# Kernel optimization log

Measured on AMD Instinct MI355X. Metric: run time of the kernel, lower is better.

Reference implementation:

```python
import jax, jax.numpy as jnp
import numpy as np

DIM = 768
HEADS = 12
DIM_HEAD = DIM // HEADS  # 64
INNER = DIM_HEAD * HEADS  # 768
HIDDEN = 4 * DIM  # 3072
N = 31  # num_patches + 1, fixed by Block (num_patches=30)
B = 512
EPS = 1e-5
MASK_VAL = -987654321.0


def layernorm(x, g, b):
    mu = jnp.mean(x, axis=-1, keepdims=True)
    var = jnp.mean(jnp.square(x - mu), axis=-1, keepdims=True)
    return (x - mu) * jax.lax.rsqrt(var + EPS) * g + b


def setup_inputs() -> dict:
    key = jax.random.key(0)
    ks = jax.random.split(key, 12)
    s = 0.02
    return {
        "x": jax.random.normal(ks[0], (B, N, DIM), jnp.float32),
        "ln1_g": jnp.ones((DIM,), jnp.float32),
        "ln1_b": jnp.zeros((DIM,), jnp.float32),
        "w_qkv": jax.random.normal(ks[1], (DIM, 3 * INNER), jnp.float32) * s,
        "scale": jnp.full((HEADS,), DIM_HEAD ** -0.5, jnp.float32),
        "w_o": jax.random.normal(ks[2], (INNER, DIM), jnp.float32) * s,
        "b_o": jnp.zeros((DIM,), jnp.float32),
        "ln2_g": jnp.ones((DIM,), jnp.float32),
        "ln2_b": jnp.zeros((DIM,), jnp.float32),
        "w1": jax.random.normal(ks[3], (DIM, HIDDEN), jnp.float32) * s,
        "b1": jnp.zeros((HIDDEN,), jnp.float32),
        "w2": jax.random.normal(ks[4], (HIDDEN, DIM), jnp.float32) * s,
        "b2": jnp.zeros((DIM,), jnp.float32),
    }


def reference(x, ln1_g, ln1_b, w_qkv, scale, w_o, b_o, ln2_g, ln2_b, w1, b1, w2, b2):
    b, n, _ = x.shape
    # --- LSA attention ---
    h = layernorm(x, ln1_g, ln1_b)
    qkv = h @ w_qkv  # [b, n, 3*inner]
    q, k, v = jnp.split(qkv, 3, axis=-1)
    def split_heads(t):
        return t.reshape(b, n, HEADS, DIM_HEAD).transpose(0, 2, 1, 3)  # b h n d
    q, k, v = split_heads(q), split_heads(k), split_heads(v)
    dots = jnp.einsum('bhid,bhjd->bhij', q, k) * scale[None, :, None, None]
    # diagonal exclusion mask (self-token masked out)
    diag = jnp.eye(n, dtype=bool)
    dots = jnp.where(diag[None, None], MASK_VAL, dots)
    attn = jax.nn.softmax(dots, axis=-1)
    out = jnp.einsum('bhij,bhjd->bhid', attn, v)
    out = out.transpose(0, 2, 1, 3).reshape(b, n, INNER)
    x = x + out @ w_o + b_o
    # --- MLP ---
    h2 = layernorm(x, ln2_g, ln2_b)
    h2 = jax.nn.gelu(h2 @ w1 + b1, approximate=False)
    x = x + h2 @ w2 + b2
    return x
```

## Files before the change

### kernel.cpp

```cpp
#include <hip/hip_runtime.h>
#include <math.h>

#define DIM 768
#define HEADS 12
#define DHEAD 64
#define NTOK 31
#define BATCH 512
#define MTOK (BATCH * NTOK)
#define HIDDEN 3072
#define QKVN 2304
#define MASK_VAL -987654321.0f

typedef short s16x8 __attribute__((ext_vector_type(8)));
typedef float f32x4 __attribute__((ext_vector_type(4)));

static __device__ __forceinline__ float bs2f(unsigned short u) {
  unsigned int x = ((unsigned int)u) << 16;
  return __builtin_bit_cast(float, x);
}
static __device__ __forceinline__ unsigned short f2bs(float f) {
  unsigned int x = __builtin_bit_cast(unsigned int, f);
  x += 0x7fffu + ((x >> 16) & 1u);
  return (unsigned short)(x >> 16);
}

static __device__ __forceinline__ void gload16(const unsigned short* g, unsigned short* l) {
  __builtin_amdgcn_global_load_lds(
      (const __attribute__((address_space(1))) unsigned int*)g,
      (__attribute__((address_space(3))) unsigned int*)l, 16, 0, 0);
}

__global__ __launch_bounds__(256) void transpose_kernel(const float* __restrict__ w,
                                                        unsigned short* __restrict__ wt,
                                                        int K, int N) {
  __shared__ float t[64][65];
  int k0 = blockIdx.y * 64, n0 = blockIdx.x * 64;
  int tid = threadIdx.x;
  int r = tid >> 4, c4 = (tid & 15) * 4;
#pragma unroll
  for (int i = 0; i < 4; ++i) {
    float4 v = *(const float4*)(w + (size_t)(k0 + r + i * 16) * N + n0 + c4);
    t[r + i * 16][c4] = v.x;
    t[r + i * 16][c4 + 1] = v.y;
    t[r + i * 16][c4 + 2] = v.z;
    t[r + i * 16][c4 + 3] = v.w;
  }
  __syncthreads();
#pragma unroll
  for (int i = 0; i < 4; ++i) {
    int n = r + i * 16;
    ushort4 o;
    o.x = f2bs(t[c4 + 0][n]);
    o.y = f2bs(t[c4 + 1][n]);
    o.z = f2bs(t[c4 + 2][n]);
    o.w = f2bs(t[c4 + 3][n]);
    *(ushort4*)(wt + (size_t)(n0 + n) * K + k0 + c4) = o;
  }
}

__global__ __launch_bounds__(256) void ln_kernel(const float* __restrict__ x,
                                                 const float* __restrict__ g,
                                                 const float* __restrict__ bta,
                                                 unsigned short* __restrict__ out) {
  int wid = threadIdx.x >> 6, lane = threadIdx.x & 63;
  size_t row = (size_t)blockIdx.x * 4 + wid;
  const float4* xr = (const float4*)(x + row * DIM);
  float4 v[3];
  v[0] = xr[lane];
  v[1] = xr[lane + 64];
  v[2] = xr[lane + 128];
  float s = 0.f, sq = 0.f;
#pragma unroll
  for (int i = 0; i < 3; ++i) {
    s += v[i].x + v[i].y + v[i].z + v[i].w;
    sq += v[i].x * v[i].x + v[i].y * v[i].y + v[i].z * v[i].z + v[i].w * v[i].w;
  }
#pragma unroll
  for (int off = 32; off; off >>= 1) {
    s += __shfl_xor(s, off);
    sq += __shfl_xor(sq, off);
  }
  float mu = s * (1.f / DIM);
  float var = sq * (1.f / DIM) - mu * mu;
  float rs = rsqrtf(var + 1e-5f);
#pragma unroll
  for (int i = 0; i < 3; ++i) {
    int col = i * 256 + lane * 4;
    float4 gg = *(const float4*)(g + col);
    float4 bb = *(const float4*)(bta + col);
    ushort4 o;
    o.x = f2bs((v[i].x - mu) * rs * gg.x + bb.x);
    o.y = f2bs((v[i].y - mu) * rs * gg.y + bb.y);
    o.z = f2bs((v[i].z - mu) * rs * gg.z + bb.z);
    o.w = f2bs((v[i].w - mu) * rs * gg.w + bb.w);
    *(ushort4*)(out + row * DIM + col) = o;
  }
}

__global__ __launch_bounds__(256) void ln_bf16_kernel(const unsigned short* __restrict__ x,
                                                      const float* __restrict__ g,
                                                      const float* __restrict__ bta,
                                                      unsigned short* __restrict__ out) {
  int wid = threadIdx.x >> 6, lane = threadIdx.x & 63;
  size_t row = (size_t)blockIdx.x * 4 + wid;
  const unsigned short* xr = x + row * DIM;
  float v[12];
#pragma unroll
  for (int i = 0; i < 3; ++i) {
    ushort4 u = *(const ushort4*)(xr + i * 256 + lane * 4);
    v[i * 4 + 0] = bs2f(u.x);
    v[i * 4 + 1] = bs2f(u.y);
    v[i * 4 + 2] = bs2f(u.z);
    v[i * 4 + 3] = bs2f(u.w);
  }
  float s = 0.f, sq = 0.f;
#pragma unroll
  for (int i = 0; i < 12; ++i) {
    s += v[i];
    sq += v[i] * v[i];
  }
#pragma unroll
  for (int off = 32; off; off >>= 1) {
    s += __shfl_xor(s, off);
    sq += __shfl_xor(sq, off);
  }
  float mu = s * (1.f / DIM);
  float var = sq * (1.f / DIM) - mu * mu;
  float rs = rsqrtf(var + 1e-5f);
#pragma unroll
  for (int i = 0; i < 3; ++i) {
    int col = i * 256 + lane * 4;
    float4 gg = *(const float4*)(g + col);
    float4 bb = *(const float4*)(bta + col);
    ushort4 o;
    o.x = f2bs((v[i * 4 + 0] - mu) * rs * gg.x + bb.x);
    o.y = f2bs((v[i * 4 + 1] - mu) * rs * gg.y + bb.y);
    o.z = f2bs((v[i * 4 + 2] - mu) * rs * gg.z + bb.z);
    o.w = f2bs((v[i * 4 + 3] - mu) * rs * gg.w + bb.w);
    *(ushort4*)(out + row * DIM + col) = o;
  }
}


template <int BUF, int MH, int KH, int VM, typename STF>
__device__ __forceinline__ void gphase(const char* aP0, const char* aP1,
                                       const char* bP0, const char* bP1,
                                       s16x8* bk, f32x4 (&acc)[8][4], STF&& stage) {
  const char* aP = BUF ? aP1 : aP0;
  const char* bP = BUF ? bP1 : bP0;
  s16x8 af[4];
  if (MH == 0) {
#pragma unroll
    for (int ni = 0; ni < 4; ++ni)
      bk[ni] = *(const s16x8*)(bP + KH * 16384 + ni * 1024);
  }
#pragma unroll
  for (int mi = 0; mi < 4; ++mi)
    af[mi] = *(const s16x8*)(aP + KH * 16384 + MH * 4096 + mi * 1024);
  stage();
  if (VM == 10) asm volatile("s_waitcnt vmcnt(10)");
  if (VM == 4) asm volatile("s_waitcnt vmcnt(4)");
  if (VM == 0) asm volatile("s_waitcnt vmcnt(0)");
  __builtin_amdgcn_s_barrier();
  asm volatile("s_waitcnt lgkmcnt(0)");
  __builtin_amdgcn_s_setprio(1);
#pragma unroll
  for (int mi = 0; mi < 4; ++mi)
#pragma unroll
    for (int ni = 0; ni < 4; ++ni)
      acc[MH * 4 + mi][ni] =
          __builtin_amdgcn_mfma_f32_16x16x32_bf16(af[mi], bk[ni], acc[MH * 4 + mi][ni], 0, 0, 0);
  __builtin_amdgcn_s_setprio(0);
  __builtin_amdgcn_s_barrier();
}

template <int EPI>
__device__ __forceinline__ void gemm8_body(
    const unsigned short* __restrict__ A, const unsigned short* __restrict__ Bt,
    void* __restrict__ outp, const float* __restrict__ bias,
    const void* __restrict__ resid, int M, int N, int K, int ntn) {
  __shared__ unsigned short lds[65536];
  const char* ldsb = (const char*)lds;
  int tid = threadIdx.x;
  int lane = tid & 63, w = tid >> 6;
  int wm = w >> 2, wn = w & 3;
  int fr = lane & 15, q = lane >> 4;

  int nwg = gridDim.x, orig = blockIdx.x;
  int qd = nwg >> 3, r8 = nwg & 7, xcd = orig & 7, loc = orig >> 3;
  int bid = (xcd < r8 ? xcd * (qd + 1) : r8 * (qd + 1) + (xcd - r8) * qd) + loc;
  int m0 = (bid / ntn) * 256, n0 = (bid % ntn) * 256;

  int rdoff = (q * 16) ^ (((fr >> 1) & 3) << 4);
  const char* aP0 = ldsb + (wm * 128 + fr) * 64 + rdoff;
  const char* aP1 = aP0 + 65536;
  const char* bP0 = ldsb + 32768 + (wn * 64 + fr) * 64 + rdoff;
  const char* bP1 = bP0 + 65536;

  int srow = tid >> 2;
  int seoff = (((tid & 3) ^ ((srow >> 1) & 3))) << 3;
  const char* Ab = (const char*)A + ((size_t)(m0 + srow) * K + seoff) * 2;
  const char* Bb = (const char*)Bt + ((size_t)(n0 + srow) * K + seoff) * 2;
  size_t rstep = (size_t)K * 256;

  auto stg = [&](int mat, int kh, int buf, int tile) {
    const char* gp = (mat ? Bb : Ab) + tile * 128 + kh * 64;
    unsigned short* lp = lds + buf * 32768 + mat * 16384 + kh * 8192 + w * 512;
    gload16((const unsigned short*)gp, lp);
    gload16((const unsigned short*)(gp + rstep), lp + 4096);
  };
  auto nop = [&] {};

  f32x4 acc[8][4] = {};
  s16x8 bk[4];
  int NT = K / 64;

  stg(1, 0, 0, 0);
  stg(0, 0, 0, 0);
  stg(1, 1, 0, 0);
  stg(0, 1, 0, 0);
  stg(1, 0, 1, 1);
  stg(0, 0, 1, 1);
  stg(1, 1, 1, 1);
  asm volatile("s_waitcnt vmcnt(6)");
  __builtin_amdgcn_s_barrier();

  for (int t = 0; t + 3 < NT; t += 2) {
    gphase<0, 0, 0, -1>(aP0, aP1, bP0, bP1, bk, acc, [&] { stg(0, 1, 1, t + 1); });
    gphase<0, 1, 0, 10>(aP0, aP1, bP0, bP1, bk, acc, [&] { stg(1, 0, 0, t + 2); });
    gphase<0, 0, 1, -1>(aP0, aP1, bP0, bP1, bk, acc, [&] { stg(0, 0, 0, t + 2); });
    gphase<0, 1, 1, 10>(aP0, aP1, bP0, bP1, bk, acc, [&] { stg(1, 1, 0, t + 2); });
    gphase<1, 0, 0, -1>(aP0, aP1, bP0, bP1, bk, acc, [&] { stg(0, 1, 0, t + 2); });
    gphase<1, 1, 0, 10>(aP0, aP1, bP0, bP1, bk, acc, [&] { stg(1, 0, 1, t + 3); });
    gphase<1, 0, 1, -1>(aP0, aP1, bP0, bP1, bk, acc, [&] { stg(0, 0, 1, t + 3); });
    gphase<1, 1, 1, 10>(aP0, aP1, bP0, bP1, bk, acc, [&] { stg(1, 1, 1, t + 3); });
  }
  gphase<0, 0, 0, -1>(aP0, aP1, bP0, bP1, bk, acc, [&] { stg(0, 1, 1, NT - 1); });
  gphase<0, 1, 0, -1>(aP0, aP1, bP0, bP1, bk, acc, nop);
  gphase<0, 0, 1, -1>(aP0, aP1, bP0, bP1, bk, acc, nop);
  gphase<0, 1, 1, 4>(aP0, aP1, bP0, bP1, bk, acc, nop);
  gphase<1, 0, 0, -1>(aP0, aP1, bP0, bP1, bk, acc, nop);
  gphase<1, 1, 0, 0>(aP0, aP1, bP0, bP1, bk, acc, nop);
  gphase<1, 0, 1, -1>(aP0, aP1, bP0, bP1, bk, acc, nop);
  gphase<1, 1, 1, -1>(aP0, aP1, bP0, bP1, bk, acc, nop);

#pragma unroll
  for (int am = 0; am < 8; ++am) {
#pragma unroll
    for (int ni = 0; ni < 4; ++ni) {
#pragma unroll
      for (int rr = 0; rr < 4; ++rr) {
        int row = m0 + wm * 128 + am * 16 + q * 4 + rr;
        int col = n0 + wn * 64 + ni * 16 + fr;
        size_t idx = (size_t)row * N + col;
        float v = acc[am][ni][rr];
        if (EPI == 0) {
          ((unsigned short*)outp)[idx] = f2bs(v);
        } else if (EPI == 2) {
          float t = v + bias[col];
          float arg = 1.5957691216f * t * (1.f + 0.044715f * t * t);
          float gl = t * __builtin_amdgcn_rcpf(1.f + __expf(-arg));
          ((unsigned short*)outp)[idx] = f2bs(gl);
        } else if (EPI == 3) {
          float t = v + bias[col] + ((const float*)resid)[idx];
          ((unsigned short*)outp)[idx] = f2bs(t);
        } else {
          float t = v + bias[col] + bs2f(((const unsigned short*)resid)[idx]);
          ((float*)outp)[idx] = t;
        }
      }
    }
  }
}

__global__ __launch_bounds__(512, 2) void gemm_qkv(const unsigned short* A,
                                                   const unsigned short* Bt, void* o,
                                                   const float* b, const void* r, int M,
                                                   int N, int K, int ntn) {
  gemm8_body<0>(A, Bt, o, b, r, M, N, K, ntn);
}
__global__ __launch_bounds__(512, 2) void gemm_proj(const unsigned short* A,
                                                    const unsigned short* Bt, void* o,
                                                    const float* b, const void* r, int M,
                                                    int N, int K, int ntn) {
  gemm8_body<3>(A, Bt, o, b, r, M, N, K, ntn);
}
__global__ __launch_bounds__(512, 2) void gemm_mlp1(const unsigned short* A,
                                                    const unsigned short* Bt, void* o,
                                                    const float* b, const void* r, int M,
                                                    int N, int K, int ntn) {
  gemm8_body<2>(A, Bt, o, b, r, M, N, K, ntn);
}
__global__ __launch_bounds__(512, 2) void gemm_mlp2(const unsigned short* A,
                                                    const unsigned short* Bt, void* o,
                                                    const float* b, const void* r, int M,
                                                    int N, int K, int ntn) {
  gemm8_body<4>(A, Bt, o, b, r, M, N, K, ntn);
}

__global__ __launch_bounds__(256) void attn_mfma_kernel(const unsigned short* __restrict__ qkv,
                                                        const float* __restrict__ scale,
                                                        unsigned short* __restrict__ ao) {
  __shared__ unsigned short Vt[4][64][40];
  __shared__ unsigned short Pl[4][32][32];
  int wid = threadIdx.x >> 6, lane = threadIdx.x & 63;
  int pair = blockIdx.x * 4 + wid;
  int b = pair / HEADS, h = pair % HEADS;
  const unsigned short* base = qkv + (size_t)b * NTOK * QKVN + h * DHEAD;
  const unsigned short* Qp = base;
  const unsigned short* Kp = base + 768;
  const unsigned short* Vp = base + 1536;

  int c = lane & 15, q = lane >> 4;
  int oct = q * 8;

  unsigned short vcol[NTOK];
#pragma unroll
  for (int j = 0; j < NTOK; ++j) vcol[j] = Vp[(size_t)j * QKVN + lane];
#pragma unroll
  for (int j = 0; j < NTOK; ++j) Vt[wid][lane][j] = vcol[j];
  Vt[wid][lane][31] = 0;

  s16x8 kf[2][2] = {{{0}}}, qf[2][2] = {{{0}}};
#pragma unroll
  for (int t = 0; t < 2; ++t) {
    int row = t * 16 + c;
    if (row < NTOK) {
#pragma unroll
      for (int s = 0; s < 2; ++s) {
        kf[t][s] = *(const s16x8*)(Kp + (size_t)row * QKVN + s * 32 + oct);
        qf[t][s] = *(const s16x8*)(Qp + (size_t)row * QKVN + s * 32 + oct);
      }
    }
  }

  f32x4 st[2][2] = {};
#pragma unroll
  for (int jt = 0; jt < 2; ++jt)
#pragma unroll
    for (int it = 0; it < 2; ++it)
#pragma unroll
      for (int s = 0; s < 2; ++s)
        st[jt][it] =
            __builtin_amdgcn_mfma_f32_16x16x32_bf16(kf[jt][s], qf[it][s], st[jt][it], 0, 0, 0);

  float scl = scale[h];
  float p[2][2][4];
#pragma unroll
  for (int it = 0; it < 2; ++it)
#pragma unroll
    for (int jt = 0; jt < 2; ++jt)
#pragma unroll
      for (int r = 0; r < 4; ++r) {
        int j = jt * 16 + 4 * q + r;
        int i = it * 16 + c;
        float v = st[jt][it][r] * scl;
        if (j == 31 || j == i) v = MASK_VAL;
        p[it][jt][r] = v;
      }
#pragma unroll
  for (int it = 0; it < 2; ++it) {
    float m = p[it][0][0];
#pragma unroll
    for (int jt = 0; jt < 2; ++jt)
#pragma unroll
      for (int r = 0; r < 4; ++r) m = fmaxf(m, p[it][jt][r]);
    m = fmaxf(m, __shfl_xor(m, 16));
    m = fmaxf(m, __shfl_xor(m, 32));
    float s = 0.f;
#pragma unroll
    for (int jt = 0; jt < 2; ++jt)
#pragma unroll
      for (int r = 0; r < 4; ++r) {
        float e = __expf(p[it][jt][r] - m);
        p[it][jt][r] = e;
        s += e;
      }
    s += __shfl_xor(s, 16);
    s += __shfl_xor(s, 32);
    float inv = __builtin_amdgcn_rcpf(s);
#pragma unroll
    for (int jt = 0; jt < 2; ++jt)
#pragma unroll
      for (int r = 0; r < 4; ++r) p[it][jt][r] *= inv;
  }
#pragma unroll
  for (int it = 0; it < 2; ++it)
#pragma unroll
    for (int jt = 0; jt < 2; ++jt) {
      unsigned int w0 =
          (unsigned int)f2bs(p[it][jt][0]) | ((unsigned int)f2bs(p[it][jt][1]) << 16);
      unsigned int w1 =
          (unsigned int)f2bs(p[it][jt][2]) | ((unsigned int)f2bs(p[it][jt][3]) << 16);
      uint2 pk = {w0, w1};
      *(uint2*)&Pl[wid][it * 16 + c][jt * 16 + 4 * q] = pk;
    }

  s16x8 pa[2];
#pragma unroll
  for (int it = 0; it < 2; ++it) pa[it] = *(const s16x8*)&Pl[wid][it * 16 + c][oct];
  f32x4 o[2][4];
#pragma unroll
  for (int it = 0; it < 2; ++it)
#pragma unroll
    for (int dt = 0; dt < 4; ++dt) {
      s16x8 vb = *(const s16x8*)&Vt[wid][dt * 16 + c][oct];
      f32x4 z = {0.f, 0.f, 0.f, 0.f};
      o[it][dt] = __builtin_amdgcn_mfma_f32_16x16x32_bf16(pa[it], vb, z, 0, 0, 0);
    }
#pragma unroll
  for (int it = 0; it < 2; ++it)
#pragma unroll
    for (int r = 0; r < 4; ++r) {
      int i = it * 16 + 4 * q + r;
      if (i < NTOK) {
        size_t rowoff = ((size_t)b * NTOK + i) * DIM + h * DHEAD;
#pragma unroll
        for (int dt = 0; dt < 4; ++dt) ao[rowoff + dt * 16 + c] = f2bs(o[it][dt][r]);
      }
    }
}

extern "C" void kernel_launch(void* const* d_in, const int* in_sizes, int n_in,
                              void* d_out, int out_size, void* d_ws, size_t ws_size,
                              hipStream_t stream) {
  (void)in_sizes; (void)n_in; (void)out_size; (void)ws_size;
  const float* x = (const float*)d_in[0];
  const float* ln1_g = (const float*)d_in[1];
  const float* ln1_b = (const float*)d_in[2];
  const float* w_qkv = (const float*)d_in[3];
  const float* scale = (const float*)d_in[4];
  const float* w_o = (const float*)d_in[5];
  const float* b_o = (const float*)d_in[6];
  const float* ln2_g = (const float*)d_in[7];
  const float* ln2_b = (const float*)d_in[8];
  const float* w1 = (const float*)d_in[9];
  const float* b1 = (const float*)d_in[10];
  const float* w2 = (const float*)d_in[11];
  const float* b2 = (const float*)d_in[12];

  char* ws = (char*)d_ws;
  unsigned short* buf1 = (unsigned short*)(ws + 0);
  unsigned short* qkv_bf = (unsigned short*)(ws + 24379392);
  unsigned short* x2 = (unsigned short*)(ws + 24379392);
  unsigned short* g_bf = (unsigned short*)(ws + 97517568);
  unsigned short* wqkvT = (unsigned short*)(ws + 195035136);
  unsigned short* woT = (unsigned short*)(ws + 198574080);
  unsigned short* w1T = (unsigned short*)(ws + 199753728);
  unsigned short* w2T = (unsigned short*)(ws + 204472320);

  transpose_kernel<<<dim3(QKVN / 64, DIM / 64), 256, 0, stream>>>(w_qkv, wqkvT, DIM, QKVN);
  transpose_kernel<<<dim3(DIM / 64, DIM / 64), 256, 0, stream>>>(w_o, woT, DIM, DIM);
  transpose_kernel<<<dim3(HIDDEN / 64, DIM / 64), 256, 0, stream>>>(w1, w1T, DIM, HIDDEN);
  transpose_kernel<<<dim3(DIM / 64, HIDDEN / 64), 256, 0, stream>>>(w2, w2T, HIDDEN, DIM);

  ln_kernel<<<MTOK / 4, 256, 0, stream>>>(x, ln1_g, ln1_b, buf1);
  gemm_qkv<<<(MTOK / 256) * (QKVN / 256), 512, 0, stream>>>(
      buf1, wqkvT, qkv_bf, nullptr, nullptr, MTOK, QKVN, DIM, QKVN / 256);
  attn_mfma_kernel<<<(BATCH * HEADS) / 4, 256, 0, stream>>>(qkv_bf, scale, buf1);
  gemm_proj<<<(MTOK / 256) * (DIM / 256), 512, 0, stream>>>(
      buf1, woT, x2, b_o, x, MTOK, DIM, DIM, DIM / 256);
  ln_bf16_kernel<<<MTOK / 4, 256, 0, stream>>>(x2, ln2_g, ln2_b, buf1);
  gemm_mlp1<<<(MTOK / 256) * (HIDDEN / 256), 512, 0, stream>>>(
      buf1, w1T, g_bf, b1, nullptr, MTOK, HIDDEN, DIM, HIDDEN / 256);
  gemm_mlp2<<<(MTOK / 256) * (DIM / 256), 512, 0, stream>>>(
      g_bf, w2T, (float*)d_out, b2, x2, MTOK, DIM, HIDDEN, DIM / 256);
}
```

Baseline: 342.3 us.

## Add 256x192 tile GEMM kernel for N=768 projection and MLP2 GEMMs

Introduces a new GEMM body with 256x192 output tiles (each of 8 waves covers 128x48) and its own LDS layout, swizzle and staging schedule. It is used for the attention output projection and the second MLP GEMM, both of which have N=768. The aim is better wave quantization across CUs: 62 M-tiles times 4 N-tiles gives 248 workgroups instead of 186. In exchange, each workgroup does less MFMA work per byte of A it loads, and the hand-tuned vmcnt wait pipeline is new and could contain stalls or errors. The epilogue code is also factored into shared helper functions.

Result: faster. 330.3 us (-3.5%).

```diff
diff --git a/kernel.cpp b/kernel.cpp
--- a/kernel.cpp
+++ b/kernel.cpp
@@ -28,6 +28,23 @@
   __builtin_amdgcn_global_load_lds(
       (const __attribute__((address_space(1))) unsigned int*)g,
       (__attribute__((address_space(3))) unsigned int*)l, 16, 0, 0);
+}
+
+static __device__ __forceinline__ float epi_apply(int EPI, float v, int col, size_t idx,
+                                                  const float* bias, const void* resid) {
+  if (EPI == 0) return v;
+  if (EPI == 2) {
+    float t = v + bias[col];
+    float arg = 1.5957691216f * t * (1.f + 0.044715f * t * t);
+    return t * __builtin_amdgcn_rcpf(1.f + __expf(-arg));
+  }
+  if (EPI == 3) return v + bias[col] + ((const float*)resid)[idx];
+  return v + bias[col] + bs2f(((const unsigned short*)resid)[idx]);
+}
+
+static __device__ __forceinline__ void epi_store(int EPI, void* outp, size_t idx, float t) {
+  if (EPI == 4) ((float*)outp)[idx] = t;
+  else ((unsigned short*)outp)[idx] = f2bs(t);
 }
 
 __global__ __launch_bounds__(256) void transpose_kernel(const float* __restrict__ w,
@@ -141,7 +158,6 @@
   }
 }
 
-
 template <int BUF, int MH, int KH, int VM, typename STF>
 __device__ __forceinline__ void gphase(const char* aP0, const char* aP1,
                                        const char* bP0, const char* bP1,
@@ -245,32 +261,134 @@
   gphase<1, 1, 1, -1>(aP0, aP1, bP0, bP1, bk, acc, nop);
 
 #pragma unroll
-  for (int am = 0; am < 8; ++am) {
-#pragma unroll
-    for (int ni = 0; ni < 4; ++ni) {
+  for (int am = 0; am < 8; ++am)
+#pragma unroll
+    for (int ni = 0; ni < 4; ++ni)
+#pragma unroll
+      for (int rr = 0; rr < 4; ++rr) {
+        int row = m0 + wm * 128 + am * 16 + (lane >> 4) * 4 + rr;
+        int col = n0 + wn * 64 + ni * 16 + fr;
+        size_t idx = (size_t)row * N + col;
+        epi_store(EPI, outp, idx, epi_apply(EPI, acc[am][ni][rr], col, idx, bias, resid));
+      }
+}
+
+template <int BUF, int MH, int KH, int VM, typename STF>
+__device__ __forceinline__ void gph192(const char* aB0, const char* bKH0, const char* bKH1,
+                                       s16x8 (&bk)[3], f32x4 (&acc)[8][3], STF&& stage) {
+  const char* aP = aB0 + BUF * 32768 + KH * 16384 + MH * 4096;
+  s16x8 af[4];
+  if (MH == 0) {
+    const char* bp = (KH ? bKH1 : bKH0) + BUF * 24576;
+#pragma unroll
+    for (int ni = 0; ni < 3; ++ni) bk[ni] = *(const s16x8*)(bp + ni * 2048);
+  }
+#pragma unroll
+  for (int mi = 0; mi < 4; ++mi) af[mi] = *(const s16x8*)(aP + mi * 1024);
+  stage();
+  if (VM == 2) asm volatile("s_waitcnt vmcnt(2)");
+  if (VM == 0) asm volatile("s_waitcnt vmcnt(0)");
+  __builtin_amdgcn_s_barrier();
+  asm volatile("s_waitcnt lgkmcnt(0)");
+  __builtin_amdgcn_s_setprio(1);
+#pragma unroll
+  for (int mi = 0; mi < 4; ++mi)
+#pragma unroll
+    for (int ni = 0; ni < 3; ++ni)
+      acc[MH * 4 + mi][ni] =
+          __builtin_amdgcn_mfma_f32_16x16x32_bf16(af[mi], bk[ni], acc[MH * 4 + mi][ni], 0, 0, 0);
+  __builtin_amdgcn_s_setprio(0);
+  __builtin_amdgcn_s_barrier();
+}
+
+template <int EPI>
+__device__ __forceinline__ void gemm192_body(
+    const unsigned short* __restrict__ A, const unsigned short* __restrict__ Bt,
+    void* __restrict__ outp, const float* __restrict__ bias,
+    const void* __restrict__ resid, int M, int N, int K, int ntn) {
+  __shared__ char ldsc[114688];
+  int tid = threadIdx.x;
+  int lane = tid & 63, w = tid >> 6;
+  int wm = w >> 2, wn = w & 3;
+  int fr = lane & 15, q = lane >> 4;
+
+  int nwg = gridDim.x, orig = blockIdx.x;
+  int qd = nwg >> 3, r8 = nwg & 7, xcd = orig & 7, loc = orig >> 3;
+  int bid = (xcd < r8 ? xcd * (qd + 1) : r8 * (qd + 1) + (xcd - r8) * qd) + loc;
+  int m0 = (bid / ntn) * 256, n0 = (bid % ntn) * 192;
+
+  int rdoffA = (q * 16) ^ (((fr >> 1) & 3) << 4);
+  const char* aB0 = ldsc + (wm * 128 + fr) * 64 + rdoffA;
+  int brow0 = wn * 48 + fr;
+  int bsw = brow0 & 7;
+  const char* bBase = ldsc + 65536 + brow0 * 128 + (q ^ (bsw & 3)) * 16;
+  const char* bKH0 = bBase + ((0 ^ (bsw >> 2)) * 64);
+  const char* bKH1 = bBase + ((1 ^ (bsw >> 2)) * 64);
+
+  int srow = tid >> 2;
+  int seoffA = (((tid & 3) ^ ((srow >> 1) & 3))) << 3;
+  const char* Ab = (const char*)A + ((size_t)(m0 + srow) * K + seoffA) * 2;
+  size_t rstep = (size_t)K * 256;
+  auto stgA = [&](int kh, int buf, int tile) {
+    const char* gp = Ab + tile * 128 + kh * 64;
+    unsigned short* lp = (unsigned short*)(ldsc + buf * 32768 + kh * 16384 + w * 1024);
+    gload16((const unsigned short*)gp, lp);
+    gload16((const unsigned short*)(gp + rstep), (unsigned short*)((char*)lp + 8192));
+  };
+  const char* Bb2 = (const char*)Bt +
+                    ((size_t)(n0 + (tid >> 3)) * K + (((tid & 7) ^ ((tid >> 3) & 7)) * 8)) * 2;
+  auto stgB = [&](int j, int buf, int tile) {
+    gload16((const unsigned short*)(Bb2 + (size_t)j * 128 * K + tile * 128),
+            (unsigned short*)(ldsc + 65536 + buf * 24576 + j * 8192 + w * 1024));
+  };
+  auto nop = [&] {};
+
+  f32x4 acc[8][3] = {};
+  s16x8 bk[3];
+  int NT = K / 64;
+
+  stgA(0, 0, 0);
+  stgA(1, 0, 0);
+  stgB(0, 0, 0);
+  stgB(1, 0, 0);
+  stgB(2, 0, 0);
+  stgA(0, 1, 1);
+  asm volatile("s_waitcnt vmcnt(2)");
+  __builtin_amdgcn_s_barrier();
+
+  for (int t = 0; t + 3 < NT; t += 2) {
+    gph192<0, 0, 0, -1>(aB0, bKH0, bKH1, bk, acc,
+                        [&] { stgA(1, 1, t + 1); stgB(0, 1, t + 1); stgB(1, 1, t + 1); });
+    gph192<0, 1, 0, -1>(aB0, bKH0, bKH1, bk, acc, [&] { stgB(2, 1, t + 1); });
+    gph192<0, 0, 1, -1>(aB0, bKH0, bKH1, bk, acc, [&] { stgA(0, 0, t + 2); });
+    gph192<0, 1, 1, 2>(aB0, bKH0, bKH1, bk, acc, nop);
+    gph192<1, 0, 0, -1>(aB0, bKH0, bKH1, bk, acc,
+                        [&] { stgA(1, 0, t + 2); stgB(0, 0, t + 2); stgB(1, 0, t + 2); });
+    gph192<1, 1, 0, -1>(aB0, bKH0, bKH1, bk, acc, [&] { stgB(2, 0, t + 2); });
+    gph192<1, 0, 1, -1>(aB0, bKH0, bKH1, bk, acc, [&] { stgA(0, 1, t + 3); });
+    gph192<1, 1, 1, 2>(aB0, bKH0, bKH1, bk, acc, nop);
+  }
+  gph192<0, 0, 0, -1>(aB0, bKH0, bKH1, bk, acc,
+                      [&] { stgA(1, 1, NT - 1); stgB(0, 1, NT - 1); stgB(1, 1, NT - 1); });
+  gph192<0, 1, 0, -1>(aB0, bKH0, bKH1, bk, acc, [&] { stgB(2, 1, NT - 1); });
+  gph192<0, 0, 1, -1>(aB0, bKH0, bKH1, bk, acc, nop);
+  gph192<0, 1, 1, 0>(aB0, bKH0, bKH1, bk, acc, nop);
+  gph192<1, 0, 0, -1>(aB0, bKH0, bKH1, bk, acc, nop);
+  gph192<1, 1, 0, -1>(aB0, bKH0, bKH1, bk, acc, nop);
+  gph192<1, 0, 1, -1>(aB0, bKH0, bKH1, bk, acc, nop);
+  gph192<1, 1, 1, -1>(aB0, bKH0, bKH1, bk, acc, nop);
+
+#pragma unroll
+  for (int am = 0; am < 8; ++am)
+#pragma unroll
+    for (int ni = 0; ni < 3; ++ni)
 #pragma unroll
       for (int rr = 0; rr < 4; ++rr) {
         int row = m0 + wm * 128 + am * 16 + q * 4 + rr;
-        int col = n0 + wn * 64 + ni * 16 + fr;
+        int col = n0 + wn * 48 + ni * 16 + fr;
         size_t idx = (size_t)row * N + col;
-        float v = acc[am][ni][rr];
-        if (EPI == 0) {
-          ((unsigned short*)outp)[idx] = f2bs(v);
-        } else if (EPI == 2) {
-          float t = v + bias[col];
-          float arg = 1.5957691216f * t * (1.f + 0.044715f * t * t);
-          float gl = t * __builtin_amdgcn_rcpf(1.f + __expf(-arg));
-          ((unsigned short*)outp)[idx] = f2bs(gl);
-        } else if (EPI == 3) {
-          float t = v + bias[col] + ((const float*)resid)[idx];
-          ((unsigned short*)outp)[idx] = f2bs(t);
-        } else {
-          float t = v + bias[col] + bs2f(((const unsigned short*)resid)[idx]);
-          ((float*)outp)[idx] = t;
-        }
+        epi_store(EPI, outp, idx, epi_apply(EPI, acc[am][ni][rr], col, idx, bias, resid));
       }
-    }
-  }
 }
 
 __global__ __launch_bounds__(512, 2) void gemm_qkv(const unsigned short* A,
@@ -279,23 +397,23 @@
                                                    int N, int K, int ntn) {
   gemm8_body<0>(A, Bt, o, b, r, M, N, K, ntn);
 }
-__global__ __launch_bounds__(512, 2) void gemm_proj(const unsigned short* A,
-                                                    const unsigned short* Bt, void* o,
-                                                    const float* b, const void* r, int M,
-                                                    int N, int K, int ntn) {
-  gemm8_body<3>(A, Bt, o, b, r, M, N, K, ntn);
-}
 __global__ __launch_bounds__(512, 2) void gemm_mlp1(const unsigned short* A,
                                                     const unsigned short* Bt, void* o,
                                                     const float* b, const void* r, int M,
                                                     int N, int K, int ntn) {
   gemm8_body<2>(A, Bt, o, b, r, M, N, K, ntn);
 }
+__global__ __launch_bounds__(512, 2) void gemm_proj(const unsigned short* A,
+                                                    const unsigned short* Bt, void* o,
+                                                    const float* b, const void* r, int M,
+                                                    int N, int K, int ntn) {
+  gemm192_body<3>(A, Bt, o, b, r, M, N, K, ntn);
+}
 __global__ __launch_bounds__(512, 2) void gemm_mlp2(const unsigned short* A,
                                                     const unsigned short* Bt, void* o,
                                                     const float* b, const void* r, int M,
                                                     int N, int K, int ntn) {
-  gemm8_body<4>(A, Bt, o, b, r, M, N, K, ntn);
+  gemm192_body<4>(A, Bt, o, b, r, M, N, K, ntn);
 }
 
 __global__ __launch_bounds__(256) void attn_mfma_kernel(const unsigned short* __restrict__ qkv,
@@ -458,11 +576,11 @@
   gemm_qkv<<<(MTOK / 256) * (QKVN / 256), 512, 0, stream>>>(
       buf1, wqkvT, qkv_bf, nullptr, nullptr, MTOK, QKVN, DIM, QKVN / 256);
   attn_mfma_kernel<<<(BATCH * HEADS) / 4, 256, 0, stream>>>(qkv_bf, scale, buf1);
-  gemm_proj<<<(MTOK / 256) * (DIM / 256), 512, 0, stream>>>(
-      buf1, woT, x2, b_o, x, MTOK, DIM, DIM, DIM / 256);
+  gemm_proj<<<(MTOK / 256) * (DIM / 192), 512, 0, stream>>>(
+      buf1, woT, x2, b_o, x, MTOK, DIM, DIM, DIM / 192);
   ln_bf16_kernel<<<MTOK / 4, 256, 0, stream>>>(x2, ln2_g, ln2_b, buf1);
   gemm_mlp1<<<(MTOK / 256) * (HIDDEN / 256), 512, 0, stream>>>(
       buf1, w1T, g_bf, b1, nullptr, MTOK, HIDDEN, DIM, HIDDEN / 256);
-  gemm_mlp2<<<(MTOK / 256) * (DIM / 256), 512, 0, stream>>>(
-      g_bf, w2T, (float*)d_out, b2, x2, MTOK, DIM, HIDDEN, DIM / 256);
-}
+  gemm_mlp2<<<(MTOK / 256) * (DIM / 192), 512, 0, stream>>>(
+      g_bf, w2T, (float*)d_out, b2, x2, MTOK, DIM, HIDDEN, DIM / 192);
+}
```
